# Optimization experiments

Measured on AMD Instinct MI355X. Metric: run time of the kernel, lower is better.

The kernel has to match this reference:

```python
import jax, jax.numpy as jnp
import numpy as np
from jax import lax

DN = ('NCHW', 'OIHW', 'NCHW')

def conv2d(x, w, b=None, padding='SAME'):
    y = lax.conv_general_dilated(x, w, (1, 1), padding, dimension_numbers=DN)
    if b is not None:
        y = y + b[None, :, None, None]
    return y

def setup_inputs() -> dict:
    key = jax.random.key(0)
    ks = jax.random.split(key, 9)
    B, C, H, W = 8, 256, 64, 64
    s = lambda fan: 1.0 / np.sqrt(fan)
    return {
        'x': jax.random.normal(ks[0], (B, C, H, W), jnp.float32),
        'qkv_w': jax.random.normal(ks[1], (3 * C, C, 1, 1), jnp.float32) * s(C),
        'qkv_b': jnp.zeros((3 * C,), jnp.float32),
        'out_w': jax.random.normal(ks[2], (C, C, 1, 1), jnp.float32) * s(C),
        'out_b': jnp.zeros((C,), jnp.float32),
        'd1_w': jax.random.normal(ks[3], (8, 1, 3, 3), jnp.float32) * s(9),
        'd1_b': jnp.zeros((8,), jnp.float32),
        'd2_w': jax.random.normal(ks[4], (1, 8, 3, 3), jnp.float32) * s(72),
        'd2_b': jnp.zeros((1,), jnp.float32),
    }

def reference(x, qkv_w, qkv_b, out_w, out_b, d1_w, d1_b, d2_w, d2_b):
    B, C, H, W = x.shape
    N = H * W
    # gradient-energy (Laplacian) density proxy
    gray = x.mean(axis=1, keepdims=True)                      # [B,1,H,W]
    lap_k = jnp.array([[0., -1., 0.], [-1., 4., -1.], [0., -1., 0.]],
                      dtype=x.dtype).reshape(1, 1, 3, 3)
    lap = conv2d(gray, lap_k)                                 # [B,1,H,W]
    h = jax.nn.relu(conv2d(jnp.abs(lap), d1_w, d1_b))         # [B,8,H,W]
    density = jax.nn.sigmoid(conv2d(h, d2_w, d2_b))           # [B,1,H,W]
    # qkv via 1x1 conv == channel matmul
    qkv = jnp.einsum('oc,bchw->bohw', qkv_w[:, :, 0, 0], x) + qkv_b[None, :, None, None]
    q, k, v = jnp.split(qkv, 3, axis=1)                       # each [B,C,H,W]
    q = q.reshape(B, C, N).transpose(0, 2, 1)                 # [B,N,C]
    k = k.reshape(B, C, N)                                    # [B,C,N]
    v = v.reshape(B, C, N).transpose(0, 2, 1)                 # [B,N,C]
    attn = jnp.einsum('bnc,bcm->bnm', q, k) * (float(C) ** -0.5)  # [B,Nq,Nk]
    temperature = 1.0 + 2.0 * (1.0 - density.reshape(B, 1, N))    # per-key [B,1,Nk]
    attn = jax.nn.softmax(attn / temperature, axis=-1)
    out = jnp.einsum('bnm,bmc->bnc', attn, v)                 # [B,N,C]
    out = out.transpose(0, 2, 1).reshape(B, C, H, W)
    out = jnp.einsum('oc,bchw->bohw', out_w[:, :, 0, 0], out) + out_b[None, :, None, None]
    return out + x
```

## Files before the change

### kernel.cpp

```cpp
#include <hip/hip_runtime.h>
#include <hip/hip_bf16.h>

typedef __attribute__((ext_vector_type(8))) short s16x8;
typedef __attribute__((ext_vector_type(4))) float f32x4;
typedef __attribute__((ext_vector_type(4))) unsigned short us4;
typedef __attribute__((ext_vector_type(4))) unsigned int u32x4;

#define MFMA16(a,b,c) __builtin_amdgcn_mfma_f32_16x16x32_bf16((a),(b),(c),0,0,0)

__device__ __forceinline__ float b2f(unsigned short u){
  union{unsigned u; float f;} v; v.u = ((unsigned)u)<<16; return v.f;
}
__device__ __forceinline__ unsigned short f2b(float f){
  union{float f; unsigned u;} v; v.f = f;
  unsigned r = v.u + 0x7fffu + ((v.u>>16)&1u);
  return (unsigned short)(r>>16);
}

__device__ __forceinline__ void gl_lds16(const void* gp, void* lp){
  __builtin_amdgcn_global_load_lds((const __attribute__((address_space(1))) void*)gp,
                                   (__attribute__((address_space(3))) void*)lp, 16, 0, 0);
}

__device__ __forceinline__ void stage_64x256(void* lds, const unsigned short* g, int stride){
  const int t = threadIdx.x, wv = t>>6;
  #pragma unroll
  for (int i=0;i<8;++i){
    int ch = i*256 + t;
    int row = ch>>5, cc = ch&31, sc = cc ^ (row&7);
    gl_lds16((const char*)(g + (size_t)row*stride) + sc*16,
             (char*)lds + (((size_t)i*256 + wv*64)<<4));
  }
}
__device__ __forceinline__ void stage_K512(void* lds, const unsigned short* g){
  const int t = threadIdx.x, wv = t>>6;
  #pragma unroll
  for (int i=0;i<4;++i){
    int ch = i*512 + t;
    int row = ch>>5, cc = ch&31, sc = cc ^ (row&7);
    gl_lds16((const char*)g + (size_t)row*512 + sc*16,
             (char*)lds + (((size_t)i*512 + wv*64)<<4));
  }
}
__device__ __forceinline__ void stage_V512(void* lds, const unsigned short* g){
  const int t = threadIdx.x, wv = t>>6;
  #pragma unroll
  for (int i=0;i<4;++i){
    int ch = i*512 + t;
    int row = ch>>3, cc = ch&7, sc = cc ^ (row&7);
    gl_lds16((const char*)(g + (size_t)row*4096) + sc*16,
             (char*)lds + (((size_t)i*512 + wv*64)<<4));
  }
}

__global__ void k_cvt(const float* __restrict__ src, unsigned short* __restrict__ dst){
  int i = blockIdx.x*256 + threadIdx.x;
  f32x4 v = *(const f32x4*)(src + (size_t)i*4);
  us4 o;
  #pragma unroll
  for (int r=0;r<4;++r) o[r] = f2b(v[r]);
  *(us4*)(dst + (size_t)i*4) = o;
}

__global__ void k_gray(const float* __restrict__ xg, float* __restrict__ gray){
  int b = blockIdx.y, n = blockIdx.x*256 + threadIdx.x;
  const float* p = xg + (size_t)b*256*4096 + n;
  float s0=0,s1=0,s2=0,s3=0;
  for (int c=0;c<256;c+=4){
    s0 += p[(size_t)c*4096];
    s1 += p[(size_t)(c+1)*4096];
    s2 += p[(size_t)(c+2)*4096];
    s3 += p[(size_t)(c+3)*4096];
  }
  gray[b*4096+n] = (s0+s1+s2+s3)*(1.f/256.f);
}

__global__ void k_lapabs(const float* __restrict__ gray, float* __restrict__ labs){
  int b = blockIdx.y, n = blockIdx.x*256 + threadIdx.x;
  int hh = n>>6, ww = n&63;
  const float* g = gray + b*4096;
  float c = g[n];
  float up = hh>0  ? g[n-64] : 0.f;
  float dn = hh<63 ? g[n+64] : 0.f;
  float lf = ww>0  ? g[n-1]  : 0.f;
  float rt = ww<63 ? g[n+1]  : 0.f;
  labs[b*4096+n] = fabsf(4.f*c - up - dn - lf - rt);
}

__global__ void k_h8(const float* __restrict__ labs, const float* __restrict__ w1,
                     const float* __restrict__ b1, float* __restrict__ hbuf){
  int b = blockIdx.y, n = blockIdx.x*256 + threadIdx.x;
  int hh = n>>6, ww = n&63;
  const float* L = labs + b*4096;
  float tap[9];
  #pragma unroll
  for (int dy=-1;dy<=1;++dy)
    #pragma unroll
    for (int dx=-1;dx<=1;++dx){
      int y=hh+dy, x2=ww+dx;
      tap[(dy+1)*3+dx+1] = (y>=0&&y<64&&x2>=0&&x2<64)? L[y*64+x2] : 0.f;
    }
  #pragma unroll
  for (int j=0;j<8;++j){
    float a = b1[j];
    #pragma unroll
    for (int k=0;k<9;++k) a += w1[j*9+k]*tap[k];
    hbuf[((size_t)(b*8+j))*4096 + n] = fmaxf(a, 0.f);
  }
}

__global__ void k_scale(const float* __restrict__ hbuf, const float* __restrict__ w2,
                        const float* __restrict__ b2_, float* __restrict__ sc){
  int b = blockIdx.y, n = blockIdx.x*256 + threadIdx.x;
  int hh = n>>6, ww = n&63;
  float a = b2_[0];
  #pragma unroll
  for (int j=0;j<8;++j){
    const float* H = hbuf + ((size_t)(b*8+j))*4096;
    #pragma unroll
    for (int dy=-1;dy<=1;++dy)
      #pragma unroll
      for (int dx=-1;dx<=1;++dx){
        int y=hh+dy, x2=ww+dx;
        if (y>=0&&y<64&&x2>=0&&x2<64) a += w2[j*9+(dy+1)*3+(dx+1)]*H[y*64+x2];
      }
  }
  float sig = 1.f/(1.f+__expf(-a));
  sc[b*4096+n] = 0.0625f/(3.f - 2.f*sig);
}

__global__ void k_transpose(const float* __restrict__ xg, unsigned short* __restrict__ Xtg){
  __shared__ unsigned short T[64*68];
  const int nb = blockIdx.x, cb = blockIdx.y, b = blockIdx.z;
  const int n0 = nb*64, c0 = cb*64;
  const int t = threadIdx.x;
  #pragma unroll
  for (int i=0;i<4;++i){
    int idx = i*256 + t;
    int c = idx>>4, k4 = idx&15;
    f32x4 v = *(const f32x4*)(xg + ((size_t)(b*256 + c0 + c))*4096 + n0 + k4*4);
    us4 o;
    #pragma unroll
    for (int r=0;r<4;++r) o[r] = f2b(v[r]);
    *(us4*)&T[c*68 + k4*4] = o;
  }
  __syncthreads();
  #pragma unroll
  for (int i=0;i<2;++i){
    int idx = i*256 + t;
    int n = idx>>3, ck = idx&7;
    unsigned short vv[8];
    #pragma unroll
    for (int j=0;j<8;++j) vv[j] = T[(ck*8+j)*68 + n];
    *(u32x4*)(Xtg + ((size_t)(b*4096 + n0 + n))*256 + c0 + ck*8) = *(const u32x4*)vv;
  }
}

__global__ __launch_bounds__(256,2) void k_gemm_qkv(const unsigned short* __restrict__ Wg,
    const unsigned short* __restrict__ Xtg, const float* __restrict__ biasg,
    unsigned short* __restrict__ Qo, unsigned short* __restrict__ Ko, unsigned short* __restrict__ Vto){
  __shared__ unsigned short Wl[64*256], Xl[64*256];
  const int nt_ = blockIdx.x, at = blockIdx.y, b = blockIdx.z;
  const int a0 = at*64, n0 = nt_*64;
  stage_64x256(Wl, Wg + (size_t)a0*256, 256);
  stage_64x256(Xl, Xtg + ((size_t)(b*4096 + n0))*256, 256);
  __syncthreads();
  const int t = threadIdx.x, w = t>>6, lane = t&63, lam = lane&15, lg = lane>>4;
  f32x4 zz = {0.f,0.f,0.f,0.f};
  f32x4 acc[4] = {zz,zz,zz,zz};
  #pragma unroll
  for (int u=0;u<8;++u){
    int ar = 16*w + lam;
    s16x8 af = *(const s16x8*)((const char*)Wl + ar*512 + ((64*u+16*lg) ^ ((ar&7)<<4)));
    #pragma unroll
    for (int ct=0;ct<4;++ct){
      int br = 16*ct + lam;
      s16x8 bf = *(const s16x8*)((const char*)Xl + br*512 + ((64*u+16*lg) ^ ((br&7)<<4)));
      acc[ct] = MFMA16(af, bf, acc[ct]);
    }
  }
  const int ob = a0 + 16*w + 4*lg;
  f32x4 bias4 = *(const f32x4*)(biasg + ob);
  #pragma unroll
  for (int ct=0;ct<4;++ct){
    int n = n0 + 16*ct + lam;
    us4 ov;
    #pragma unroll
    for (int r=0;r<4;++r) ov[r] = f2b(acc[ct][r] + bias4[r]);
    if (a0 < 256){
      *(us4*)(Qo + ((size_t)(b*4096 + n))*256 + ob) = ov;
    } else if (a0 < 512){
      *(us4*)(Ko + ((size_t)(b*4096 + n))*256 + (ob-256)) = ov;
    } else {
      #pragma unroll
      for (int r=0;r<4;++r)
        Vto[((size_t)(b*256 + (ob-512+r)))*4096 + n] = ov[r];
    }
  }
}

__global__ __launch_bounds__(512,2) void k_attn(const unsigned short* __restrict__ Qg,
    const unsigned short* __restrict__ Kg, const unsigned short* __restrict__ Vtg,
    const float* __restrict__ Sg, unsigned short* __restrict__ AOt){
  __shared__ unsigned short Kl[2][64*256];
  __shared__ unsigned short Vl[2][256*64];
  __shared__ __align__(16) unsigned short Pl[8][16*64];

  const int t = threadIdx.x, w = t>>6, lane = t&63, lam = lane&15, lg = lane>>4;
  const int bid = blockIdx.x;
  const int b = bid&7, qt = bid>>3;
  const int qbase = qt*128 + w*16;

  s16x8 qf[8];
  {
    const unsigned short* qp = Qg + ((size_t)(b*4096 + qbase + lam))*256 + lg*8;
    #pragma unroll
    for (int u=0;u<8;++u) qf[u] = *(const s16x8*)(qp + 32*u);
  }
  f32x4 zz = {0.f,0.f,0.f,0.f};
  f32x4 oa[16];
  #pragma unroll
  for (int i=0;i<16;++i) oa[i] = zz;
  float m_run = -1.0e30f, l_run = 0.f;

  const unsigned short* Kb = Kg + (size_t)b*4096*256;
  const unsigned short* Vb = Vtg + (size_t)b*256*4096;

  stage_K512(&Kl[0][0], Kb);
  stage_V512(&Vl[0][0], Vb);
  __syncthreads();

  int cur = 0;
  for (int kt=0; kt<64; ++kt){
    const int m0 = kt*64;
    if (kt < 63){
      stage_K512(&Kl[cur^1][0], Kb + (size_t)(m0+64)*256);
      stage_V512(&Vl[cur^1][0], Vb + (m0+64));
    }
    f32x4 s4[4];
    #pragma unroll
    for (int mt=0;mt<4;++mt) s4[mt] = *(const f32x4*)(Sg + (size_t)b*4096 + m0 + 16*mt + 4*lg);

    f32x4 st[4] = {zz,zz,zz,zz};
    const char* Kc = (const char*)&Kl[cur][0];
    __builtin_amdgcn_s_setprio(1);
    #pragma unroll
    for (int u=0;u<8;++u){
      #pragma unroll
      for (int mt=0;mt<4;++mt){
        int krow = 16*mt + lam;
        s16x8 kf = *(const s16x8*)(Kc + krow*512 + ((64*u + 16*lg) ^ ((krow&7)<<4)));
        st[mt] = MFMA16(kf, qf[u], st[mt]);
      }
    }
    __builtin_amdgcn_s_setprio(0);

    float tmax = -1.0e30f;
    #pragma unroll
    for (int mt=0;mt<4;++mt){
      #pragma unroll
      for (int r=0;r<4;++r){ st[mt][r] *= s4[mt][r]; tmax = fmaxf(tmax, st[mt][r]); }
    }
    tmax = fmaxf(tmax, __shfl_xor(tmax,16));
    tmax = fmaxf(tmax, __shfl_xor(tmax,32));
    float mnew = fmaxf(m_run, tmax);
    float fs = __expf(m_run - mnew);
    float rsum = 0.f;
    #pragma unroll
    for (int mt=0;mt<4;++mt){
      #pragma unroll
      for (int r=0;r<4;++r){ float e = __expf(st[mt][r]-mnew); st[mt][r]=e; rsum += e; }
    }
    rsum += __shfl_xor(rsum,16);
    rsum += __shfl_xor(rsum,32);
    l_run = l_run*fs + rsum; m_run = mnew;

    #pragma unroll
    for (int mt=0;mt<4;++mt){
      us4 pk;
      #pragma unroll
      for (int r=0;r<4;++r) pk[r] = f2b(st[mt][r]);
      *(us4*)((char*)&Pl[w][0] + lam*128 + ((mt*32 + lg*8) ^ ((lam&7)<<4))) = pk;
    }
    float fr[4];
    #pragma unroll
    for (int r=0;r<4;++r) fr[r] = __shfl(fs, 4*lg + r);
    #pragma unroll
    for (int i=0;i<16;++i){
      #pragma unroll
      for (int r=0;r<4;++r) oa[i][r] *= fr[r];
    }
    const char* Vc = (const char*)&Vl[cur][0];
    __builtin_amdgcn_s_setprio(1);
    #pragma unroll
    for (int ks=0;ks<2;++ks){
      s16x8 pa = *(const s16x8*)((const char*)&Pl[w][0] + lam*128 + ((ks*64 + lg*16) ^ ((lam&7)<<4)));
      #pragma unroll
      for (int ct=0;ct<16;++ct){
        int c = lam + 16*ct;
        s16x8 vf = *(const s16x8*)(Vc + c*128 + ((ks*64 + 16*lg) ^ ((c&7)<<4)));
        oa[ct] = MFMA16(pa, vf, oa[ct]);
      }
    }
    __builtin_amdgcn_s_setprio(0);

    __syncthreads();
    cur ^= 1;
  }
  float li = 1.f/l_run;
  float lr[4];
  #pragma unroll
  for (int r=0;r<4;++r) lr[r] = __shfl(li, 4*lg + r);
  #pragma unroll
  for (int ct=0;ct<16;++ct){
    #pragma unroll
    for (int r=0;r<4;++r){
      AOt[((size_t)(b*4096 + qbase + 4*lg + r))*256 + lam + 16*ct] = f2b(oa[ct][r]*lr[r]);
    }
  }
}

__global__ __launch_bounds__(256,2) void k_gemm_out(const unsigned short* __restrict__ Ag,
    const unsigned short* __restrict__ Bg, const float* __restrict__ biasg,
    const float* __restrict__ xg, float* __restrict__ outg){
  __shared__ unsigned short Al[64*256], Bl[64*256];
  const int at = blockIdx.x, bt = blockIdx.y, b = blockIdx.z;
  const int a0 = at*64, o0 = bt*64;
  stage_64x256(Al, Ag + ((size_t)(b*4096 + a0))*256, 256);
  stage_64x256(Bl, Bg + (size_t)o0*256, 256);
  __syncthreads();
  const int t = threadIdx.x, w = t>>6, lane = t&63, lam = lane&15, lg = lane>>4;
  f32x4 zz = {0.f,0.f,0.f,0.f};
  f32x4 acc[4] = {zz,zz,zz,zz};
  #pragma unroll
  for (int u=0;u<8;++u){
    int ar = 16*w + lam;
    s16x8 af = *(const s16x8*)((const char*)Al + ar*512 + ((64*u+16*lg) ^ ((ar&7)<<4)));
    #pragma unroll
    for (int ct=0;ct<4;++ct){
      int br = 16*ct + lam;
      s16x8 bf = *(const s16x8*)((const char*)Bl + br*512 + ((64*u+16*lg) ^ ((br&7)<<4)));
      acc[ct] = MFMA16(af, bf, acc[ct]);
    }
  }
  #pragma unroll
  for (int ct=0;ct<4;++ct){
    int o = o0 + 16*ct + lam;
    float ob_ = biasg[o];
    size_t base = ((size_t)(b*256 + o))*4096 + a0 + 16*w + 4*lg;
    f32x4 xv = *(const f32x4*)(xg + base);
    f32x4 ov;
    #pragma unroll
    for (int r=0;r<4;++r) ov[r] = acc[ct][r] + ob_ + xv[r];
    *(f32x4*)(outg + base) = ov;
  }
}

extern "C" void kernel_launch(void* const* d_in, const int* in_sizes, int n_in,
                              void* d_out, int out_size, void* d_ws, size_t ws_size,
                              hipStream_t stream){
  const float* x     = (const float*)d_in[0];
  const float* qkv_w = (const float*)d_in[1];
  const float* qkv_b = (const float*)d_in[2];
  const float* out_w = (const float*)d_in[3];
  const float* out_b = (const float*)d_in[4];
  const float* d1_w  = (const float*)d_in[5];
  const float* d1_b  = (const float*)d_in[6];
  const float* d2_w  = (const float*)d_in[7];
  const float* d2_b  = (const float*)d_in[8];
  float* out = (float*)d_out;

  char* p = (char*)d_ws;
  const size_t BIG = (size_t)8*4096*256*2;
  unsigned short* Xt = (unsigned short*)p; p += BIG;
  unsigned short* Q  = (unsigned short*)p; p += BIG;
  unsigned short* K  = (unsigned short*)p; p += BIG;
  unsigned short* Vt = (unsigned short*)p; p += BIG;
  unsigned short* Wq = (unsigned short*)p; p += (size_t)768*256*2;
  unsigned short* Wo = (unsigned short*)p; p += (size_t)256*256*2;
  float* gray = (float*)p; p += (size_t)8*4096*4;
  float* labs = (float*)p; p += (size_t)8*4096*4;
  float* hbuf = (float*)p; p += (size_t)8*8*4096*4;
  float* sc   = (float*)p; p += (size_t)8*4096*4;

  k_cvt      <<<dim3(192),    256, 0, stream>>>(qkv_w, Wq);
  k_cvt      <<<dim3(64),     256, 0, stream>>>(out_w, Wo);
  k_transpose<<<dim3(64,4,8), 256, 0, stream>>>(x, Xt);
  k_gray     <<<dim3(16,8),   256, 0, stream>>>(x, gray);
  k_lapabs   <<<dim3(16,8),   256, 0, stream>>>(gray, labs);
  k_h8       <<<dim3(16,8),   256, 0, stream>>>(labs, d1_w, d1_b, hbuf);
  k_scale    <<<dim3(16,8),   256, 0, stream>>>(hbuf, d2_w, d2_b, sc);
  k_gemm_qkv <<<dim3(64,12,8),256, 0, stream>>>(Wq, Xt, qkv_b, Q, K, Vt);
  k_attn     <<<dim3(256),    512, 0, stream>>>(Q, K, Vt, sc, Xt);
  k_gemm_out <<<dim3(64,4,8), 256, 0, stream>>>(Xt, Wo, out_b, x, out);
}
```

Baseline: 325.8 us.

## Switch attention to 32x32x16 MFMA with 4 waves of 32 query rows

The flash-attention kernel moves from 16x16x32 MFMA tiles with 8 waves of 16 query rows each to 32x32x16 MFMA tiles with 4 waves of 32 query rows each. The block drops to 256 threads and the launch bounds change to one block per SIMD group. Each K and V fragment read from LDS now feeds twice as many query rows, which cuts LDS traffic per flop, and the softmax reductions need fewer cross-lane shuffles. In exchange, the accumulators use far more registers (8x16 floats for O plus the S tiles), and fewer waves are available to hide latency. The staging helpers are rewritten to load the same tiles with 256 threads.

```diff
diff --git a/kernel.cpp b/kernel.cpp
--- a/kernel.cpp
+++ b/kernel.cpp
@@ -3,10 +3,12 @@
 
 typedef __attribute__((ext_vector_type(8))) short s16x8;
 typedef __attribute__((ext_vector_type(4))) float f32x4;
+typedef __attribute__((ext_vector_type(16))) float f32x16;
 typedef __attribute__((ext_vector_type(4))) unsigned short us4;
 typedef __attribute__((ext_vector_type(4))) unsigned int u32x4;
 
 #define MFMA16(a,b,c) __builtin_amdgcn_mfma_f32_16x16x32_bf16((a),(b),(c),0,0,0)
+#define MFMA32(a,b,c) __builtin_amdgcn_mfma_f32_32x32x16_bf16((a),(b),(c),0,0,0)
 
 __device__ __forceinline__ float b2f(unsigned short u){
   union{unsigned u; float f;} v; v.u = ((unsigned)u)<<16; return v.f;
@@ -32,24 +34,14 @@
              (char*)lds + (((size_t)i*256 + wv*64)<<4));
   }
 }
-__device__ __forceinline__ void stage_K512(void* lds, const unsigned short* g){
+__device__ __forceinline__ void stage_256x64(void* lds, const unsigned short* g){
   const int t = threadIdx.x, wv = t>>6;
   #pragma unroll
-  for (int i=0;i<4;++i){
-    int ch = i*512 + t;
-    int row = ch>>5, cc = ch&31, sc = cc ^ (row&7);
-    gl_lds16((const char*)g + (size_t)row*512 + sc*16,
-             (char*)lds + (((size_t)i*512 + wv*64)<<4));
-  }
-}
-__device__ __forceinline__ void stage_V512(void* lds, const unsigned short* g){
-  const int t = threadIdx.x, wv = t>>6;
-  #pragma unroll
-  for (int i=0;i<4;++i){
-    int ch = i*512 + t;
+  for (int i=0;i<8;++i){
+    int ch = i*256 + t;
     int row = ch>>3, cc = ch&7, sc = cc ^ (row&7);
     gl_lds16((const char*)(g + (size_t)row*4096) + sc*16,
-             (char*)lds + (((size_t)i*512 + wv*64)<<4));
+             (char*)lds + (((size_t)i*256 + wv*64)<<4));
   }
 }
 
@@ -199,107 +191,129 @@
   }
 }
 
-__global__ __launch_bounds__(512,2) void k_attn(const unsigned short* __restrict__ Qg,
+__global__ __launch_bounds__(256,1) void k_attn(const unsigned short* __restrict__ Qg,
     const unsigned short* __restrict__ Kg, const unsigned short* __restrict__ Vtg,
     const float* __restrict__ Sg, unsigned short* __restrict__ AOt){
   __shared__ unsigned short Kl[2][64*256];
   __shared__ unsigned short Vl[2][256*64];
-  __shared__ __align__(16) unsigned short Pl[8][16*64];
-
-  const int t = threadIdx.x, w = t>>6, lane = t&63, lam = lane&15, lg = lane>>4;
+  __shared__ __align__(16) unsigned short Pl[4][32*64];
+
+  const int t = threadIdx.x, w = t>>6, lane = t&63, l31 = lane&31, h = lane>>5;
   const int bid = blockIdx.x;
   const int b = bid&7, qt = bid>>3;
-  const int qbase = qt*128 + w*16;
-
-  s16x8 qf[8];
+  const int qbase = qt*128 + w*32;
+
+  s16x8 qf[16];
   {
-    const unsigned short* qp = Qg + ((size_t)(b*4096 + qbase + lam))*256 + lg*8;
-    #pragma unroll
-    for (int u=0;u<8;++u) qf[u] = *(const s16x8*)(qp + 32*u);
-  }
-  f32x4 zz = {0.f,0.f,0.f,0.f};
-  f32x4 oa[16];
-  #pragma unroll
-  for (int i=0;i<16;++i) oa[i] = zz;
+    const unsigned short* qp = Qg + ((size_t)(b*4096 + qbase + l31))*256 + 8*h;
+    #pragma unroll
+    for (int u=0;u<16;++u) qf[u] = *(const s16x8*)(qp + 16*u);
+  }
+  f32x16 st0, st1, oa[8];
+  #pragma unroll
+  for (int i=0;i<16;++i){ st0[i]=0.f; st1[i]=0.f; }
+  #pragma unroll
+  for (int nb=0;nb<8;++nb)
+    #pragma unroll
+    for (int i=0;i<16;++i) oa[nb][i]=0.f;
   float m_run = -1.0e30f, l_run = 0.f;
 
   const unsigned short* Kb = Kg + (size_t)b*4096*256;
   const unsigned short* Vb = Vtg + (size_t)b*256*4096;
-
-  stage_K512(&Kl[0][0], Kb);
-  stage_V512(&Vl[0][0], Vb);
+  const float* Sb = Sg + (size_t)b*4096;
+
+  stage_64x256(&Kl[0][0], Kb, 256);
+  stage_256x64(&Vl[0][0], Vb);
   __syncthreads();
 
   int cur = 0;
   for (int kt=0; kt<64; ++kt){
     const int m0 = kt*64;
     if (kt < 63){
-      stage_K512(&Kl[cur^1][0], Kb + (size_t)(m0+64)*256);
-      stage_V512(&Vl[cur^1][0], Vb + (m0+64));
-    }
-    f32x4 s4[4];
-    #pragma unroll
-    for (int mt=0;mt<4;++mt) s4[mt] = *(const f32x4*)(Sg + (size_t)b*4096 + m0 + 16*mt + 4*lg);
-
-    f32x4 st[4] = {zz,zz,zz,zz};
+      stage_64x256(&Kl[cur^1][0], Kb + (size_t)(m0+64)*256, 256);
+      stage_256x64(&Vl[cur^1][0], Vb + (m0+64));
+    }
     const char* Kc = (const char*)&Kl[cur][0];
+    const char* Vc = (const char*)&Vl[cur][0];
+
+    #pragma unroll
+    for (int i=0;i<16;++i){ st0[i]=0.f; st1[i]=0.f; }
     __builtin_amdgcn_s_setprio(1);
     #pragma unroll
-    for (int u=0;u<8;++u){
-      #pragma unroll
-      for (int mt=0;mt<4;++mt){
-        int krow = 16*mt + lam;
-        s16x8 kf = *(const s16x8*)(Kc + krow*512 + ((64*u + 16*lg) ^ ((krow&7)<<4)));
-        st[mt] = MFMA16(kf, qf[u], st[mt]);
+    for (int u=0;u<16;++u){
+      int off = (32*u + 16*h) ^ ((l31&7)<<4);
+      s16x8 kf0 = *(const s16x8*)(Kc + l31*512 + off);
+      s16x8 kf1 = *(const s16x8*)(Kc + (32+l31)*512 + off);
+      st0 = MFMA32(kf0, qf[u], st0);
+      st1 = MFMA32(kf1, qf[u], st1);
+    }
+    __builtin_amdgcn_s_setprio(0);
+
+    float pm[32];
+    {
+      #pragma unroll
+      for (int j=0;j<4;++j){
+        f32x4 sv = *(const f32x4*)(Sb + m0 + 8*j + 4*h);
+        #pragma unroll
+        for (int i=0;i<4;++i) pm[4*j+i] = st0[4*j+i]*sv[i];
       }
-    }
-    __builtin_amdgcn_s_setprio(0);
-
-    float tmax = -1.0e30f;
-    #pragma unroll
-    for (int mt=0;mt<4;++mt){
-      #pragma unroll
-      for (int r=0;r<4;++r){ st[mt][r] *= s4[mt][r]; tmax = fmaxf(tmax, st[mt][r]); }
-    }
-    tmax = fmaxf(tmax, __shfl_xor(tmax,16));
-    tmax = fmaxf(tmax, __shfl_xor(tmax,32));
+      #pragma unroll
+      for (int j=0;j<4;++j){
+        f32x4 sv = *(const f32x4*)(Sb + m0 + 32 + 8*j + 4*h);
+        #pragma unroll
+        for (int i=0;i<4;++i) pm[16+4*j+i] = st1[4*j+i]*sv[i];
+      }
+    }
+    float mx[16];
+    #pragma unroll
+    for (int i=0;i<16;++i) mx[i] = fmaxf(pm[i], pm[16+i]);
+    #pragma unroll
+    for (int i=0;i<8;++i) mx[i] = fmaxf(mx[i], mx[8+i]);
+    #pragma unroll
+    for (int i=0;i<4;++i) mx[i] = fmaxf(mx[i], mx[4+i]);
+    float tmax = fmaxf(fmaxf(mx[0],mx[1]), fmaxf(mx[2],mx[3]));
+    tmax = fmaxf(tmax, __shfl_xor(tmax, 32));
     float mnew = fmaxf(m_run, tmax);
     float fs = __expf(m_run - mnew);
-    float rsum = 0.f;
-    #pragma unroll
-    for (int mt=0;mt<4;++mt){
-      #pragma unroll
-      for (int r=0;r<4;++r){ float e = __expf(st[mt][r]-mnew); st[mt][r]=e; rsum += e; }
-    }
-    rsum += __shfl_xor(rsum,16);
-    rsum += __shfl_xor(rsum,32);
+    float sm[16];
+    #pragma unroll
+    for (int i=0;i<32;++i) pm[i] = __expf(pm[i]-mnew);
+    #pragma unroll
+    for (int i=0;i<16;++i) sm[i] = pm[i] + pm[16+i];
+    #pragma unroll
+    for (int i=0;i<8;++i) sm[i] += sm[8+i];
+    #pragma unroll
+    for (int i=0;i<4;++i) sm[i] += sm[4+i];
+    float rsum = (sm[0]+sm[1]) + (sm[2]+sm[3]);
+    rsum += __shfl_xor(rsum, 32);
     l_run = l_run*fs + rsum; m_run = mnew;
 
     #pragma unroll
-    for (int mt=0;mt<4;++mt){
-      us4 pk;
-      #pragma unroll
-      for (int r=0;r<4;++r) pk[r] = f2b(st[mt][r]);
-      *(us4*)((char*)&Pl[w][0] + lam*128 + ((mt*32 + lg*8) ^ ((lam&7)<<4))) = pk;
-    }
-    float fr[4];
-    #pragma unroll
-    for (int r=0;r<4;++r) fr[r] = __shfl(fs, 4*lg + r);
-    #pragma unroll
-    for (int i=0;i<16;++i){
-      #pragma unroll
-      for (int r=0;r<4;++r) oa[i][r] *= fr[r];
-    }
-    const char* Vc = (const char*)&Vl[cur][0];
+    for (int j=0;j<4;++j){
+      us4 pk0, pk1;
+      #pragma unroll
+      for (int i=0;i<4;++i){ pk0[i] = f2b(pm[4*j+i]); pk1[i] = f2b(pm[16+4*j+i]); }
+      char* base = (char*)&Pl[w][0] + l31*128;
+      *(us4*)(base + ((16*j + 8*h) ^ ((l31&7)<<4))) = pk0;
+      *(us4*)(base + ((64 + 16*j + 8*h) ^ ((l31&7)<<4))) = pk1;
+    }
+    float fr[16];
+    #pragma unroll
+    for (int r=0;r<16;++r) fr[r] = __shfl(fs, (r&3)+8*(r>>2)+4*h);
+    #pragma unroll
+    for (int nb=0;nb<8;++nb)
+      #pragma unroll
+      for (int r=0;r<16;++r) oa[nb][r] *= fr[r];
+
     __builtin_amdgcn_s_setprio(1);
     #pragma unroll
-    for (int ks=0;ks<2;++ks){
-      s16x8 pa = *(const s16x8*)((const char*)&Pl[w][0] + lam*128 + ((ks*64 + lg*16) ^ ((lam&7)<<4)));
-      #pragma unroll
-      for (int ct=0;ct<16;++ct){
-        int c = lam + 16*ct;
-        s16x8 vf = *(const s16x8*)(Vc + c*128 + ((ks*64 + 16*lg) ^ ((c&7)<<4)));
-        oa[ct] = MFMA16(pa, vf, oa[ct]);
+    for (int ks=0;ks<4;++ks){
+      s16x8 pa = *(const s16x8*)((const char*)&Pl[w][0] + l31*128 + ((32*ks + 16*h) ^ ((l31&7)<<4)));
+      #pragma unroll
+      for (int nb=0;nb<8;++nb){
+        int c = 32*nb + l31;
+        s16x8 vf = *(const s16x8*)(Vc + c*128 + ((32*ks + 16*h) ^ ((c&7)<<4)));
+        oa[nb] = MFMA32(pa, vf, oa[nb]);
       }
     }
     __builtin_amdgcn_s_setprio(0);
@@ -308,14 +322,15 @@
     cur ^= 1;
   }
   float li = 1.f/l_run;
-  float lr[4];
-  #pragma unroll
-  for (int r=0;r<4;++r) lr[r] = __shfl(li, 4*lg + r);
-  #pragma unroll
-  for (int ct=0;ct<16;++ct){
-    #pragma unroll
-    for (int r=0;r<4;++r){
-      AOt[((size_t)(b*4096 + qbase + 4*lg + r))*256 + lam + 16*ct] = f2b(oa[ct][r]*lr[r]);
+  float lr[16];
+  #pragma unroll
+  for (int r=0;r<16;++r) lr[r] = __shfl(li, (r&3)+8*(r>>2)+4*h);
+  #pragma unroll
+  for (int nb=0;nb<8;++nb){
+    #pragma unroll
+    for (int r=0;r<16;++r){
+      int qr = (r&3)+8*(r>>2)+4*h;
+      AOt[((size_t)(b*4096 + qbase + qr))*256 + 32*nb + l31] = f2b(oa[nb][r]*lr[r]);
     }
   }
 }
@@ -391,6 +406,6 @@
   k_h8       <<<dim3(16,8),   256, 0, stream>>>(labs, d1_w, d1_b, hbuf);
   k_scale    <<<dim3(16,8),   256, 0, stream>>>(hbuf, d2_w, d2_b, sc);
   k_gemm_qkv <<<dim3(64,12,8),256, 0, stream>>>(Wq, Xt, qkv_b, Q, K, Vt);
-  k_attn     <<<dim3(256),    512, 0, stream>>>(Q, K, Vt, sc, Xt);
+  k_attn     <<<dim3(256),    256, 0, stream>>>(Q, K, Vt, sc, Xt);
   k_gemm_out <<<dim3(64,4,8), 256, 0, stream>>>(Xt, Wo, out_b, x, out);
 }
```

After: 377.1 us. +15.7%, slower.
